# Optimization experiments

Hardware: AMD Instinct MI355X
Metric: run time of the kernel (lower is better)

Reference implementation:

```python
import jax, jax.numpy as jnp
import numpy as np

B, S, DMODEL = 1, 2048, 4096
H, HKV, DH = 32, 8, 128
LTAB, RBKT = 20, 128
NEG = -1e9


def rotate_half(x):
    x1, x2 = x[..., : x.shape[-1] // 2], x[..., x.shape[-1] // 2:]
    return jnp.concatenate((-x2, x1), axis=-1)


def setup_inputs() -> dict:
    key = jax.random.key(0)
    ks = jax.random.split(key, 12)
    inp = {
        "hidden_states": jax.random.normal(ks[0], (B, S, DMODEL), jnp.float32),
        "cos": jax.random.uniform(ks[1], (B, S, DH), jnp.float32),
        "sin": jax.random.uniform(ks[2], (B, S, DH), jnp.float32),
        "q_probs": jax.random.uniform(ks[3], (B, H, LTAB, RBKT), jnp.float32),
        "v_norm": jax.random.uniform(ks[4], (B, H, S), jnp.float32),
        "allowed": jnp.ones((B, H, S), dtype=bool),
        "k_hard": jax.random.randint(ks[5], (B, H, LTAB, S), 0, RBKT, jnp.int32),
        "Wq": jax.random.normal(ks[6], (DMODEL, H * DH), jnp.float32) * 0.02,
        "Wk": jax.random.normal(ks[7], (DMODEL, HKV * DH), jnp.float32) * 0.02,
        "Wv": jax.random.normal(ks[8], (DMODEL, HKV * DH), jnp.float32) * 0.02,
        "Wo": jax.random.normal(ks[9], (H * DH, DMODEL), jnp.float32) * 0.02,
        "sink": 4,
        "window": 128,
        "M": 256,
    }
    return inp


def _sparse_key_mask(q_probs, v_norm, allowed, k_hard, sink, window, M):
    """Faithful jax version of build_sparse_list_decode, returned as a boolean
    allowed-key mask [B, H, T] (equivalent to scattering sparse_list)."""
    Bm, Hm, _, T = k_hard.shape
    # soft-hash collision score: sum over tables of q bucket prob at key's bucket,
    # weighted by value-norm history, restricted to allowed keys.
    coll = jnp.take_along_axis(q_probs, k_hard.astype(jnp.int32), axis=-1).sum(axis=2)  # [B,H,T]
    scores = jnp.where(allowed, coll * v_norm, -jnp.inf)
    M_eff = min(M, T)
    mask = jnp.zeros((Bm, Hm, T), dtype=bool)
    if M_eff > 0:
        heavy_idx = jax.lax.top_k(scores, M_eff)[1]  # [B,H,M]
        b_ix = jnp.arange(Bm)[:, None, None]
        h_ix = jnp.arange(Hm)[None, :, None]
        mask = mask.at[b_ix, h_ix, heavy_idx].set(True)
    sink = max(0, min(sink, T))
    window = max(0, min(window, T))
    if sink > 0:
        mask = mask.at[:, :, :sink].set(True)
    if window > 0:
        win_start = max(T - window, sink)
        if win_start < T:
            mask = mask.at[:, :, win_start:].set(True)
    if sink == 0 and window == 0:
        mask = mask.at[:, :, T - 1].set(True)
    return mask & allowed


def reference(hidden_states, cos, sin, q_probs, v_norm, allowed, k_hard,
              Wq, Wk, Wv, Wo, sink, window, M):
    Bx, Sx, _ = hidden_states.shape
    scaling = DH ** -0.5
    q = (hidden_states @ Wq).reshape(Bx, Sx, H, DH).transpose(0, 2, 1, 3)   # [B,H,S,Dh]
    k = (hidden_states @ Wk).reshape(Bx, Sx, HKV, DH).transpose(0, 2, 1, 3)  # [B,Hkv,S,Dh]
    v = (hidden_states @ Wv).reshape(Bx, Sx, HKV, DH).transpose(0, 2, 1, 3)
    # RoPE (unsqueeze_dim=1)
    c, s = cos[:, None, :, :], sin[:, None, :, :]
    q = q * c + rotate_half(q) * s
    k = k * c + rotate_half(k) * s
    # repeat_kv for GQA
    n_rep = H // HKV
    k = jnp.repeat(k, n_rep, axis=1)
    v = jnp.repeat(v, n_rep, axis=1)
    # sparse heavy-hitter + sink + window key mask (no_grad in the original)
    key_mask = _sparse_key_mask(q_probs, v_norm, allowed, k_hard, sink, window, M)  # [B,H,S]
    causal = jnp.tril(jnp.ones((Sx, Sx), dtype=bool))
    allow = causal[None, None] & key_mask[:, :, None, :]  # [B,H,S,S]
    scores = jnp.einsum('bhqd,bhkd->bhqk', q, k) * scaling
    attn = jax.nn.softmax(jnp.where(allow, scores, NEG), axis=-1)
    out = jnp.einsum('bhqk,bhkd->bhqd', attn, v)
    out = out.transpose(0, 2, 1, 3).reshape(Bx, Sx, H * DH)
    return out @ Wo
```

## Files before the change

### kernel.cpp

```cpp
#include <hip/hip_runtime.h>
#include <hip/hip_bf16.h>
#include <cstdint>
#include <cstddef>

namespace {

constexpr int S_LEN = 2048;
constexpr int DM    = 4096;
constexpr int NH    = 32;
constexpr int NKV   = 8;
constexpr int DH    = 128;
constexpr int LTAB  = 20;
constexpr int RBKT  = 128;
constexpr int NQKV  = NH * DH + 2 * NKV * DH;
constexpr int KOFF  = NH * DH;
constexpr int VOFF  = NH * DH + NKV * DH;

typedef short s16x8 __attribute__((ext_vector_type(8)));
typedef float f32x4 __attribute__((ext_vector_type(4)));
typedef unsigned long long u64;
struct u64x2 { u64 x, y; };

__device__ inline short bf16s(float f) {
  __hip_bfloat16 b = __float2bfloat16(f);
  return (short)*reinterpret_cast<unsigned short*>(&b);
}
__device__ inline float s2f(short s) {
  unsigned short u = (unsigned short)s;
  return __bfloat162float(*reinterpret_cast<__hip_bfloat16*>(&u));
}

__global__ __launch_bounds__(256) void prep_kernel(const float* __restrict__ hidden,
                                                   const float* __restrict__ Wq,
                                                   const float* __restrict__ Wk,
                                                   const float* __restrict__ Wv,
                                                   const float* __restrict__ Wo,
                                                   __hip_bfloat16* __restrict__ hbf,
                                                   __hip_bfloat16* __restrict__ WqkvT,
                                                   __hip_bfloat16* __restrict__ WoT) {
  __shared__ float tile[64][65];
  const int b = blockIdx.x, tid = threadIdx.x;
  if (b < 2048) {
    const size_t base = (size_t)b * 1024;
#pragma unroll
    for (int it = 0; it < 4; ++it) {
      const size_t i = base + it * 256 + tid;
      float4 v = reinterpret_cast<const float4*>(hidden)[i];
      ushort4 o;
      o.x = (unsigned short)bf16s(v.x);
      o.y = (unsigned short)bf16s(v.y);
      o.z = (unsigned short)bf16s(v.z);
      o.w = (unsigned short)bf16s(v.w);
      reinterpret_cast<ushort4*>(hbf)[i] = o;
    }
    return;
  }
  const float* W;
  __hip_bfloat16* Wt;
  int N, bx, by;
  int t = b - 2048;
  if (t < 4096) {
    W = Wq; Wt = WqkvT; N = DM; bx = t & 63; by = t >> 6;
  } else if (t < 5120) {
    t -= 4096; W = Wk; Wt = WqkvT + (size_t)KOFF * DM; N = NKV * DH; bx = t & 15; by = t >> 4;
  } else if (t < 6144) {
    t -= 5120; W = Wv; Wt = WqkvT + (size_t)VOFF * DM; N = NKV * DH; bx = t & 15; by = t >> 4;
  } else {
    t -= 6144; W = Wo; Wt = WoT; N = DM; bx = t & 63; by = t >> 6;
  }
  const int K = DM;
  const int kb = by * 64, nb = bx * 64;
  const int r0 = tid >> 4, c4 = (tid & 15) * 4;
#pragma unroll
  for (int it = 0; it < 4; ++it) {
    const int r = r0 + it * 16;
    float4 v = *reinterpret_cast<const float4*>(&W[(size_t)(kb + r) * N + nb + c4]);
    tile[r][c4] = v.x;
    tile[r][c4 + 1] = v.y;
    tile[r][c4 + 2] = v.z;
    tile[r][c4 + 3] = v.w;
  }
  __syncthreads();
  const int n0 = tid >> 4, k4 = (tid & 15) * 4;
#pragma unroll
  for (int it = 0; it < 4; ++it) {
    const int n = n0 + it * 16;
    ushort4 o;
    o.x = (unsigned short)bf16s(tile[k4][n]);
    o.y = (unsigned short)bf16s(tile[k4 + 1][n]);
    o.z = (unsigned short)bf16s(tile[k4 + 2][n]);
    o.w = (unsigned short)bf16s(tile[k4 + 3][n]);
    *reinterpret_cast<ushort4*>(&Wt[(size_t)(nb + n) * K + kb + k4]) = o;
  }
}

template <bool OUT_F32>
__global__ __launch_bounds__(256) void gemm_bt(const __hip_bfloat16* __restrict__ A,
                                               const __hip_bfloat16* __restrict__ Bt,
                                               void* __restrict__ Cout,
                                               int N, int K) {
  __shared__ __hip_bfloat16 As[128 * 64];
  __shared__ __hip_bfloat16 Bs[128 * 64];
  const int tid = threadIdx.x;
  const int wid = tid >> 6;
  const int lane = tid & 63;
  const int bm = blockIdx.y, bn = blockIdx.x;
  const int wr = wid >> 1, wc = wid & 1;
  f32x4 acc[4][4] = {};
  const __hip_bfloat16* Abase = A + (size_t)bm * 128 * K;
  const __hip_bfloat16* Bbase = Bt + (size_t)bn * 128 * K;
  for (int kt = 0; kt < K; kt += 64) {
    __syncthreads();
#pragma unroll
    for (int j = 0; j < 4; ++j) {
      const int pb = j * 4096 + wid * 1024;
      const int p = pb + lane * 16;
      const int row = p >> 7;
      const int slot = ((p >> 4) & 7) ^ (row & 7);
      const int goff = row * K + kt + slot * 8;
      __builtin_amdgcn_global_load_lds(
          (const __attribute__((address_space(1))) void*)(Abase + goff),
          (__attribute__((address_space(3))) void*)(As + (pb >> 1)), 16, 0, 0);
      __builtin_amdgcn_global_load_lds(
          (const __attribute__((address_space(1))) void*)(Bbase + goff),
          (__attribute__((address_space(3))) void*)(Bs + (pb >> 1)), 16, 0, 0);
    }
    __syncthreads();
#pragma unroll
    for (int kk = 0; kk < 2; ++kk) {
      s16x8 af[4], bf[4];
#pragma unroll
      for (int i = 0; i < 4; ++i) {
        const int ra = wr * 64 + i * 16 + (lane & 15);
        const int sa = (kk * 4 + (lane >> 4)) ^ (ra & 7);
        af[i] = *reinterpret_cast<const s16x8*>(As + ra * 64 + sa * 8);
        const int rb = wc * 64 + i * 16 + (lane & 15);
        const int sb = (kk * 4 + (lane >> 4)) ^ (rb & 7);
        bf[i] = *reinterpret_cast<const s16x8*>(Bs + rb * 64 + sb * 8);
      }
#pragma unroll
      for (int i = 0; i < 4; ++i)
#pragma unroll
        for (int jn = 0; jn < 4; ++jn)
          acc[i][jn] = __builtin_amdgcn_mfma_f32_16x16x32_bf16(af[i], bf[jn], acc[i][jn], 0, 0, 0);
    }
  }
  const int rg = (lane >> 4) * 4;
  const int cg = lane & 15;
#pragma unroll
  for (int i = 0; i < 4; ++i)
#pragma unroll
    for (int jn = 0; jn < 4; ++jn)
#pragma unroll
      for (int r = 0; r < 4; ++r) {
        const int rr = bm * 128 + wr * 64 + i * 16 + rg + r;
        const int cc = bn * 128 + wc * 64 + jn * 16 + cg;
        if (OUT_F32)
          reinterpret_cast<float*>(Cout)[(size_t)rr * N + cc] = acc[i][jn][r];
        else
          reinterpret_cast<__hip_bfloat16*>(Cout)[(size_t)rr * N + cc] =
              __float2bfloat16(acc[i][jn][r]);
      }
}

__global__ __launch_bounds__(256) void rope_kernel(const __hip_bfloat16* __restrict__ QKV,
                                                   const float* __restrict__ cosb,
                                                   const float* __restrict__ sinb,
                                                   __hip_bfloat16* __restrict__ Qro,
                                                   __hip_bfloat16* __restrict__ Kro) {
  const int s = blockIdx.x;
  const int tid = threadIdx.x;
  const float* cs = cosb + s * DH;
  const float* sn = sinb + s * DH;
  const __hip_bfloat16* row = QKV + (size_t)s * NQKV;
  for (int ch = tid; ch < 512 + 128; ch += 256) {
    const bool isQ = ch < 512;
    const int idx8 = (isQ ? ch : ch - 512) * 8;
    const int d8 = idx8 & (DH - 1);
    const int hb = idx8 - d8;
    const __hip_bfloat16* src = isQ ? row : row + KOFF;
    s16x8 v = *reinterpret_cast<const s16x8*>(src + idx8);
    s16x8 p = *reinterpret_cast<const s16x8*>(src + hb + (d8 ^ 64));
    const float sgn = (d8 < 64) ? -1.f : 1.f;
    s16x8 outv;
#pragma unroll
    for (int j = 0; j < 8; ++j) {
      const float r = s2f(v[j]) * cs[d8 + j] + sgn * s2f(p[j]) * sn[d8 + j];
      outv[j] = bf16s(r);
    }
    if (isQ)
      *reinterpret_cast<s16x8*>(Qro + (size_t)s * (NH * DH) + idx8) = outv;
    else
      *reinterpret_cast<s16x8*>(Kro + (size_t)s * (NKV * DH) + idx8) = outv;
  }
}

__global__ __launch_bounds__(1024) void select_kernel(const float* __restrict__ q_probs,
                                                      const float* __restrict__ v_norm,
                                                      const int* __restrict__ allowed,
                                                      const int* __restrict__ k_hard,
                                                      const int* __restrict__ sinkp,
                                                      const int* __restrict__ winp,
                                                      const int* __restrict__ Mp,
                                                      int* __restrict__ sel_idx,
                                                      int* __restrict__ sel_cnt) {
  const int h = blockIdx.x;
  const int tid = threadIdx.x;
  const int lane = tid & 63;
  const int wid = tid >> 6;
  __shared__ u64 keys[S_LEN];
  __shared__ int waveTot[16];
  const int t0 = tid * 2;
  float c0 = 0.f, c1 = 0.f;
#pragma unroll
  for (int l = 0; l < LTAB; ++l) {
    const int2 kh = *reinterpret_cast<const int2*>(&k_hard[(size_t)(h * LTAB + l) * S_LEN + t0]);
    c0 += q_probs[(h * LTAB + l) * RBKT + kh.x];
    c1 += q_probs[(h * LTAB + l) * RBKT + kh.y];
  }
  const int2 al = *reinterpret_cast<const int2*>(&allowed[h * S_LEN + t0]);
  const float2 vn = *reinterpret_cast<const float2*>(&v_norm[h * S_LEN + t0]);
  const float s0 = al.x ? c0 * vn.x : -INFINITY;
  const float s1 = al.y ? c1 * vn.y : -INFINITY;
  auto mkkey = [](float s, int t) -> u64 {
    unsigned m = __float_as_uint(s);
    m = (m & 0x80000000u) ? ~m : (m | 0x80000000u);
    return ((u64)m << 11) | (u64)(S_LEN - 1 - t);
  };
  const u64 k0 = mkkey(s0, t0);
  const u64 k1 = mkkey(s1, t0 + 1);
  keys[t0] = k0;
  keys[t0 + 1] = k1;
  __syncthreads();
  int r0 = 0, r1 = 0;
#pragma unroll 8
  for (int u = 0; u < S_LEN; u += 2) {
    const u64x2 kv = *reinterpret_cast<const u64x2*>(&keys[u]);
    r0 += (kv.x > k0) + (kv.y > k0);
    r1 += (kv.x > k1) + (kv.y > k1);
  }
  const int Mv = min(Mp[0], S_LEN);
  int sv = sinkp[0];
  sv = sv < 0 ? 0 : (sv > S_LEN ? S_LEN : sv);
  int wv = winp[0];
  wv = wv < 0 ? 0 : (wv > S_LEN ? S_LEN : wv);
  int wstart = S_LEN - wv;
  if (wstart < sv) wstart = sv;
  bool sel0 = r0 < Mv, sel1 = r1 < Mv;
  if (t0 < sv) sel0 = true;
  if (t0 + 1 < sv) sel1 = true;
  if (wv > 0) {
    if (t0 >= wstart) sel0 = true;
    if (t0 + 1 >= wstart) sel1 = true;
  }
  if (sv == 0 && wv == 0) {
    if (t0 == S_LEN - 1) sel0 = true;
    if (t0 + 1 == S_LEN - 1) sel1 = true;
  }
  sel0 = sel0 && (al.x != 0);
  sel1 = sel1 && (al.y != 0);
  const int cnt = (sel0 ? 1 : 0) + (sel1 ? 1 : 0);
  int inc = cnt;
#pragma unroll
  for (int off = 1; off < 64; off <<= 1) {
    int n = __shfl_up(inc, off);
    if (lane >= off) inc += n;
  }
  if (lane == 63) waveTot[wid] = inc;
  __syncthreads();
  int wbase = 0;
  for (int w = 0; w < wid; ++w) wbase += waveTot[w];
  int pos = wbase + inc - cnt;
  if (tid == 0) {
    int tot = 0;
#pragma unroll
    for (int w = 0; w < 16; ++w) tot += waveTot[w];
    sel_cnt[h] = tot;
  }
  if (sel0) sel_idx[h * S_LEN + pos++] = t0;
  if (sel1) sel_idx[h * S_LEN + pos] = t0 + 1;
}

__global__ __launch_bounds__(256) void attn_kernel(const __hip_bfloat16* __restrict__ Qro,
                                                   const __hip_bfloat16* __restrict__ Kro,
                                                   const __hip_bfloat16* __restrict__ Vpk,
                                                   const int* __restrict__ sel_idx,
                                                   const int* __restrict__ sel_cnt,
                                                   __hip_bfloat16* __restrict__ ctx) {
  constexpr int BKV = 64;
  const int h = blockIdx.y;
  const int q0 = blockIdx.x * 64;
  const int tid = threadIdx.x, wid = tid >> 6, lane = tid & 63;
  const int l15 = lane & 15, hi = lane >> 4;
  const int kv = h >> 2;
  __shared__ __hip_bfloat16 Ks[BKV][DH + 8];
  __shared__ __hip_bfloat16 Vt[DH][BKV + 8];
  __shared__ __hip_bfloat16 Ps[4][16][BKV + 8];
  __shared__ int tIdx[BKV];
  const int qbase = q0 + wid * 16;
  const float scaling = 0.08838834764831845f;
  s16x8 qf[4];
  {
    const __hip_bfloat16* qp =
        Qro + (size_t)(qbase + l15) * (NH * DH) + h * DH + hi * 8;
#pragma unroll
    for (int kt = 0; kt < 4; ++kt) {
      s16x8 q = *reinterpret_cast<const s16x8*>(qp + kt * 32);
#pragma unroll
      for (int j = 0; j < 8; ++j) q[j] = bf16s(s2f(q[j]) * scaling);
      qf[kt] = q;
    }
  }
  s16x8 ones;
#pragma unroll
  for (int j = 0; j < 8; ++j) ones[j] = (short)0x3F80;
  float mr[4], lr[4];
#pragma unroll
  for (int r = 0; r < 4; ++r) {
    mr[r] = -3.0e38f;
    lr[r] = 0.f;
  }
  f32x4 o[8] = {};
  const int cnt = sel_cnt[h];
  const int qmax = q0 + 63;
  for (int j0 = 0; j0 < cnt; j0 += BKV) {
    if (sel_idx[h * S_LEN + j0] > qmax) break;
    const int nk = min(BKV, cnt - j0);
    __syncthreads();
    if (tid < BKV) tIdx[tid] = (tid < nk) ? sel_idx[h * S_LEN + j0 + tid] : 0x7fffffff;
#pragma unroll
    for (int c = 0; c < 4; ++c) {
      const int ch = tid + c * 256;
      const int row = ch >> 4, c8 = ch & 15;
      if (row < nk) {
        const int t = sel_idx[h * S_LEN + j0 + row];
        *reinterpret_cast<s16x8*>(&Ks[row][c8 * 8]) = *reinterpret_cast<const s16x8*>(
            Kro + (size_t)t * (NKV * DH) + kv * DH + c8 * 8);
      }
    }
    {
      const int j = tid >> 2;
      const int dp = (tid & 3) * 32;
      const int ccA = j ^ (((dp >> 4) & 7) << 3);
      const int ccB = j ^ ((((dp >> 4) + 1) & 7) << 3);
      if (j < nk) {
        const int t = sel_idx[h * S_LEN + j0 + j];
        const __hip_bfloat16* vp = Vpk + (size_t)t * NQKV + kv * DH + dp;
        s16x8 a = *reinterpret_cast<const s16x8*>(vp);
        s16x8 bq = *reinterpret_cast<const s16x8*>(vp + 8);
        s16x8 cq = *reinterpret_cast<const s16x8*>(vp + 16);
        s16x8 dq = *reinterpret_cast<const s16x8*>(vp + 24);
#pragma unroll
        for (int i = 0; i < 8; ++i) reinterpret_cast<short&>(Vt[dp + i][ccA]) = a[i];
#pragma unroll
        for (int i = 0; i < 8; ++i) reinterpret_cast<short&>(Vt[dp + 8 + i][ccA]) = bq[i];
#pragma unroll
        for (int i = 0; i < 8; ++i) reinterpret_cast<short&>(Vt[dp + 16 + i][ccB]) = cq[i];
#pragma unroll
        for (int i = 0; i < 8; ++i) reinterpret_cast<short&>(Vt[dp + 24 + i][ccB]) = dq[i];
      } else {
#pragma unroll
        for (int i = 0; i < 16; ++i) reinterpret_cast<short&>(Vt[dp + i][ccA]) = 0;
#pragma unroll
        for (int i = 0; i < 16; ++i) reinterpret_cast<short&>(Vt[dp + 16 + i][ccB]) = 0;
      }
    }
    __syncthreads();
    f32x4 sc[4];
#pragma unroll
    for (int kc = 0; kc < 4; ++kc) sc[kc] = f32x4{0.f, 0.f, 0.f, 0.f};
#pragma unroll
    for (int kt = 0; kt < 4; ++kt) {
#pragma unroll
      for (int kc = 0; kc < 4; ++kc) {
        const s16x8 kf =
            *reinterpret_cast<const s16x8*>(&Ks[kc * 16 + l15][kt * 32 + hi * 8]);
        sc[kc] = __builtin_amdgcn_mfma_f32_16x16x32_bf16(qf[kt], kf, sc[kc], 0, 0, 0);
      }
    }
    int tt[4];
#pragma unroll
    for (int kc = 0; kc < 4; ++kc) tt[kc] = tIdx[kc * 16 + l15];
    float vv[4][4];
    bool need = false;
#pragma unroll
    for (int r = 0; r < 4; ++r) {
      const int qs = qbase + (hi << 2) + r;
      float mx = -3.0e38f;
#pragma unroll
      for (int kc = 0; kc < 4; ++kc) {
        vv[kc][r] = (tt[kc] <= qs) ? sc[kc][r] : -1.0e9f;
        mx = fmaxf(mx, vv[kc][r]);
      }
      need = need || (mx > mr[r] + 8.f);
    }
    if (__any(need)) {
#pragma unroll
      for (int r = 0; r < 4; ++r) {
        float m = fmaxf(fmaxf(vv[0][r], vv[1][r]), fmaxf(vv[2][r], vv[3][r]));
#pragma unroll
        for (int off = 1; off < 16; off <<= 1) m = fmaxf(m, __shfl_xor(m, off));
        const float mn = fmaxf(mr[r], m);
        const float scl = __expf(mr[r] - mn);
        lr[r] *= scl;
#pragma unroll
        for (int nt = 0; nt < 8; ++nt) o[nt][r] *= scl;
        mr[r] = mn;
      }
    }
#pragma unroll
    for (int r = 0; r < 4; ++r) {
#pragma unroll
      for (int kc = 0; kc < 4; ++kc) {
        Ps[wid][(hi << 2) + r][kc * 16 + l15] = __float2bfloat16(__expf(vv[kc][r] - mr[r]));
      }
    }
    const s16x8 pf0 = *reinterpret_cast<const s16x8*>(&Ps[wid][l15][hi * 8]);
    const s16x8 pf1 = *reinterpret_cast<const s16x8*>(&Ps[wid][l15][32 + hi * 8]);
    {
      f32x4 zero = {0.f, 0.f, 0.f, 0.f};
      f32x4 ps = __builtin_amdgcn_mfma_f32_16x16x32_bf16(pf0, ones, zero, 0, 0, 0);
      ps = __builtin_amdgcn_mfma_f32_16x16x32_bf16(pf1, ones, ps, 0, 0, 0);
#pragma unroll
      for (int r = 0; r < 4; ++r) lr[r] += ps[r];
    }
#pragma unroll
    for (int nt = 0; nt < 8; ++nt) {
      const s16x8 vfa =
          *reinterpret_cast<const s16x8*>(&Vt[nt * 16 + l15][(hi * 8) ^ (nt * 8)]);
      const s16x8 vfb =
          *reinterpret_cast<const s16x8*>(&Vt[nt * 16 + l15][(32 + hi * 8) ^ (nt * 8)]);
      o[nt] = __builtin_amdgcn_mfma_f32_16x16x32_bf16(pf0, vfa, o[nt], 0, 0, 0);
      o[nt] = __builtin_amdgcn_mfma_f32_16x16x32_bf16(pf1, vfb, o[nt], 0, 0, 0);
    }
  }
#pragma unroll
  for (int nt = 0; nt < 8; ++nt)
#pragma unroll
    for (int r = 0; r < 4; ++r) {
      const int qs = qbase + (hi << 2) + r;
      const int d = nt * 16 + l15;
      ctx[(size_t)qs * (NH * DH) + h * DH + d] = __float2bfloat16(o[nt][r] / lr[r]);
    }
}

}

extern "C" void kernel_launch(void* const* d_in, const int* in_sizes, int n_in,
                              void* d_out, int out_size, void* d_ws, size_t ws_size,
                              hipStream_t stream) {
  const float* hidden = (const float*)d_in[0];
  const float* cosb = (const float*)d_in[1];
  const float* sinb = (const float*)d_in[2];
  const float* q_probs = (const float*)d_in[3];
  const float* v_norm = (const float*)d_in[4];
  const int* allowed = (const int*)d_in[5];
  const int* k_hard = (const int*)d_in[6];
  const float* Wq = (const float*)d_in[7];
  const float* Wk = (const float*)d_in[8];
  const float* Wv = (const float*)d_in[9];
  const float* Wo = (const float*)d_in[10];
  const int* sinkp = (const int*)d_in[11];
  const int* winp = (const int*)d_in[12];
  const int* Mp = (const int*)d_in[13];

  char* ws = (char*)d_ws;
  size_t off = 0;
  auto alloc = [&](size_t bytes) -> char* {
    char* p = ws + off;
    off += (bytes + 255) & ~(size_t)255;
    return p;
  };
  __hip_bfloat16* hbf = (__hip_bfloat16*)alloc((size_t)S_LEN * DM * 2);
  __hip_bfloat16* WqkvT = (__hip_bfloat16*)alloc((size_t)NQKV * DM * 2);
  __hip_bfloat16* WoT = (__hip_bfloat16*)alloc((size_t)DM * DM * 2);
  __hip_bfloat16* QKV = (__hip_bfloat16*)alloc((size_t)S_LEN * NQKV * 2);
  __hip_bfloat16* Qro = (__hip_bfloat16*)alloc((size_t)S_LEN * NH * DH * 2);
  __hip_bfloat16* Kro = (__hip_bfloat16*)alloc((size_t)S_LEN * NKV * DH * 2);
  __hip_bfloat16* ctx = (__hip_bfloat16*)alloc((size_t)S_LEN * NH * DH * 2);
  int* sel_idx = (int*)alloc((size_t)NH * S_LEN * 4);
  int* sel_cnt = (int*)alloc((size_t)NH * 4);
  if (off > ws_size) return;

  prep_kernel<<<12288, 256, 0, stream>>>(hidden, Wq, Wk, Wv, Wo, hbf, WqkvT, WoT);

  gemm_bt<false><<<dim3(NQKV / 128, S_LEN / 128), 256, 0, stream>>>(
      hbf, WqkvT, (void*)QKV, NQKV, DM);

  rope_kernel<<<S_LEN, 256, 0, stream>>>(QKV, cosb, sinb, Qro, Kro);

  select_kernel<<<NH, 1024, 0, stream>>>(q_probs, v_norm, allowed, k_hard, sinkp, winp, Mp,
                                         sel_idx, sel_cnt);

  attn_kernel<<<dim3(S_LEN / 64, NH), 256, 0, stream>>>(Qro, Kro, QKV + VOFF, sel_idx,
                                                        sel_cnt, ctx);

  gemm_bt<true><<<dim3(DM / 128, S_LEN / 128), 256, 0, stream>>>(ctx, WoT, d_out, DM, DM);
}
```

Measured before the change: 387.7 us.

## Fuse top-k selection into prep kernel and split-K the output projection

The per-head heavy-hitter selection moves into extra blocks of the prep kernel, with 8 keys per thread in 256-thread blocks, so the separate select launch goes away and the selection overlaps the weight conversion. The output projection GEMM becomes a two-way split-K kernel that writes fp32 partials into the workspace region of the no-longer-needed hidden and QKV weight buffers. A reduce kernel then sums the partials. This doubles the block count for the final GEMM to improve occupancy, at the cost of writing and re-reading 64MB of partials.

Result: no change. 385.6 us (-0.5%).

```diff
diff --git a/kernel.cpp b/kernel.cpp
--- a/kernel.cpp
+++ b/kernel.cpp
@@ -30,18 +30,98 @@
   return __bfloat162float(*reinterpret_cast<__hip_bfloat16*>(&u));
 }
 
-__global__ __launch_bounds__(256) void prep_kernel(const float* __restrict__ hidden,
-                                                   const float* __restrict__ Wq,
-                                                   const float* __restrict__ Wk,
-                                                   const float* __restrict__ Wv,
-                                                   const float* __restrict__ Wo,
-                                                   __hip_bfloat16* __restrict__ hbf,
-                                                   __hip_bfloat16* __restrict__ WqkvT,
-                                                   __hip_bfloat16* __restrict__ WoT) {
+__global__ __launch_bounds__(256) void prep_kernel(
+    const float* __restrict__ hidden, const float* __restrict__ Wq,
+    const float* __restrict__ Wk, const float* __restrict__ Wv,
+    const float* __restrict__ Wo, __hip_bfloat16* __restrict__ hbf,
+    __hip_bfloat16* __restrict__ WqkvT, __hip_bfloat16* __restrict__ WoT,
+    const float* __restrict__ q_probs, const float* __restrict__ v_norm,
+    const int* __restrict__ allowed, const int* __restrict__ k_hard,
+    const int* __restrict__ sinkp, const int* __restrict__ winp,
+    const int* __restrict__ Mp, int* __restrict__ sel_idx, int* __restrict__ sel_cnt) {
   __shared__ float tile[64][65];
+  __shared__ u64 keys[S_LEN];
+  __shared__ int waveTot[4];
   const int b = blockIdx.x, tid = threadIdx.x;
-  if (b < 2048) {
-    const size_t base = (size_t)b * 1024;
+  if (b < 32) {
+    const int h = b;
+    const int lane = tid & 63, wv4 = tid >> 6;
+    const int t0 = tid * 8;
+    float cs[8] = {0.f, 0.f, 0.f, 0.f, 0.f, 0.f, 0.f, 0.f};
+#pragma unroll
+    for (int l = 0; l < LTAB; ++l) {
+      const int* kb = &k_hard[(size_t)(h * LTAB + l) * S_LEN + t0];
+      const int4 ka = *reinterpret_cast<const int4*>(kb);
+      const int4 kc = *reinterpret_cast<const int4*>(kb + 4);
+      const float* qp = &q_probs[(h * LTAB + l) * RBKT];
+      cs[0] += qp[ka.x]; cs[1] += qp[ka.y]; cs[2] += qp[ka.z]; cs[3] += qp[ka.w];
+      cs[4] += qp[kc.x]; cs[5] += qp[kc.y]; cs[6] += qp[kc.z]; cs[7] += qp[kc.w];
+    }
+    const int4 alA = *reinterpret_cast<const int4*>(&allowed[h * S_LEN + t0]);
+    const int4 alB = *reinterpret_cast<const int4*>(&allowed[h * S_LEN + t0 + 4]);
+    const float4 vnA = *reinterpret_cast<const float4*>(&v_norm[h * S_LEN + t0]);
+    const float4 vnB = *reinterpret_cast<const float4*>(&v_norm[h * S_LEN + t0 + 4]);
+    const int al[8] = {alA.x, alA.y, alA.z, alA.w, alB.x, alB.y, alB.z, alB.w};
+    const float vn[8] = {vnA.x, vnA.y, vnA.z, vnA.w, vnB.x, vnB.y, vnB.z, vnB.w};
+    auto mkkey = [](float s, int t) -> u64 {
+      unsigned m = __float_as_uint(s);
+      m = (m & 0x80000000u) ? ~m : (m | 0x80000000u);
+      return ((u64)m << 11) | (u64)(S_LEN - 1 - t);
+    };
+    u64 kk[8];
+#pragma unroll
+    for (int c = 0; c < 8; ++c) {
+      const float sc = al[c] ? cs[c] * vn[c] : -INFINITY;
+      kk[c] = mkkey(sc, t0 + c);
+      keys[t0 + c] = kk[c];
+    }
+    __syncthreads();
+    int rk[8] = {0, 0, 0, 0, 0, 0, 0, 0};
+#pragma unroll 4
+    for (int u = 0; u < S_LEN; u += 2) {
+      const u64x2 kv = *reinterpret_cast<const u64x2*>(&keys[u]);
+#pragma unroll
+      for (int c = 0; c < 8; ++c) rk[c] += (kv.x > kk[c]) + (kv.y > kk[c]);
+    }
+    const int Mv = min(Mp[0], S_LEN);
+    int sv = sinkp[0];
+    sv = sv < 0 ? 0 : (sv > S_LEN ? S_LEN : sv);
+    int wvv = winp[0];
+    wvv = wvv < 0 ? 0 : (wvv > S_LEN ? S_LEN : wvv);
+    int wstart = S_LEN - wvv;
+    if (wstart < sv) wstart = sv;
+    bool sel[8];
+    int cnt = 0;
+#pragma unroll
+    for (int c = 0; c < 8; ++c) {
+      const int t = t0 + c;
+      bool s = rk[c] < Mv;
+      if (t < sv) s = true;
+      if (wvv > 0 && t >= wstart) s = true;
+      if (sv == 0 && wvv == 0 && t == S_LEN - 1) s = true;
+      s = s && (al[c] != 0);
+      sel[c] = s;
+      cnt += s ? 1 : 0;
+    }
+    int inc = cnt;
+#pragma unroll
+    for (int off = 1; off < 64; off <<= 1) {
+      int n = __shfl_up(inc, off);
+      if (lane >= off) inc += n;
+    }
+    if (lane == 63) waveTot[wv4] = inc;
+    __syncthreads();
+    int wbase = 0;
+    for (int w = 0; w < wv4; ++w) wbase += waveTot[w];
+    int pos = wbase + inc - cnt;
+    if (tid == 0) sel_cnt[h] = waveTot[0] + waveTot[1] + waveTot[2] + waveTot[3];
+#pragma unroll
+    for (int c = 0; c < 8; ++c)
+      if (sel[c]) sel_idx[h * S_LEN + pos++] = t0 + c;
+    return;
+  }
+  if (b < 32 + 2048) {
+    const size_t base = (size_t)(b - 32) * 1024;
 #pragma unroll
     for (int it = 0; it < 4; ++it) {
       const size_t i = base + it * 256 + tid;
@@ -58,7 +138,7 @@
   const float* W;
   __hip_bfloat16* Wt;
   int N, bx, by;
-  int t = b - 2048;
+  int t = b - 2080;
   if (t < 4096) {
     W = Wq; Wt = WqkvT; N = DM; bx = t & 63; by = t >> 6;
   } else if (t < 5120) {
@@ -161,6 +241,85 @@
           reinterpret_cast<__hip_bfloat16*>(Cout)[(size_t)rr * N + cc] =
               __float2bfloat16(acc[i][jn][r]);
       }
+}
+
+__global__ __launch_bounds__(256) void gemm_bt_splitk(const __hip_bfloat16* __restrict__ A,
+                                                      const __hip_bfloat16* __restrict__ Bt,
+                                                      float* __restrict__ P,
+                                                      int N, int Kfull, int KH) {
+  __shared__ __hip_bfloat16 As[128 * 64];
+  __shared__ __hip_bfloat16 Bs[128 * 64];
+  const int tid = threadIdx.x;
+  const int wid = tid >> 6;
+  const int lane = tid & 63;
+  const int bm = blockIdx.y, bn = blockIdx.x, kz = blockIdx.z;
+  const int wr = wid >> 1, wc = wid & 1;
+  f32x4 acc[4][4] = {};
+  const __hip_bfloat16* Abase = A + (size_t)bm * 128 * Kfull + kz * KH;
+  const __hip_bfloat16* Bbase = Bt + (size_t)bn * 128 * Kfull + kz * KH;
+  for (int kt = 0; kt < KH; kt += 64) {
+    __syncthreads();
+#pragma unroll
+    for (int j = 0; j < 4; ++j) {
+      const int pb = j * 4096 + wid * 1024;
+      const int p = pb + lane * 16;
+      const int row = p >> 7;
+      const int slot = ((p >> 4) & 7) ^ (row & 7);
+      const int goff = row * Kfull + kt + slot * 8;
+      __builtin_amdgcn_global_load_lds(
+          (const __attribute__((address_space(1))) void*)(Abase + goff),
+          (__attribute__((address_space(3))) void*)(As + (pb >> 1)), 16, 0, 0);
+      __builtin_amdgcn_global_load_lds(
+          (const __attribute__((address_space(1))) void*)(Bbase + goff),
+          (__attribute__((address_space(3))) void*)(Bs + (pb >> 1)), 16, 0, 0);
+    }
+    __syncthreads();
+#pragma unroll
+    for (int kk = 0; kk < 2; ++kk) {
+      s16x8 af[4], bf[4];
+#pragma unroll
+      for (int i = 0; i < 4; ++i) {
+        const int ra = wr * 64 + i * 16 + (lane & 15);
+        const int sa = (kk * 4 + (lane >> 4)) ^ (ra & 7);
+        af[i] = *reinterpret_cast<const s16x8*>(As + ra * 64 + sa * 8);
+        const int rb = wc * 64 + i * 16 + (lane & 15);
+        const int sb = (kk * 4 + (lane >> 4)) ^ (rb & 7);
+        bf[i] = *reinterpret_cast<const s16x8*>(Bs + rb * 64 + sb * 8);
+      }
+#pragma unroll
+      for (int i = 0; i < 4; ++i)
+#pragma unroll
+        for (int jn = 0; jn < 4; ++jn)
+          acc[i][jn] = __builtin_amdgcn_mfma_f32_16x16x32_bf16(af[i], bf[jn], acc[i][jn], 0, 0, 0);
+    }
+  }
+  float* Pz = P + (size_t)kz * S_LEN * N;
+  const int rg = (lane >> 4) * 4;
+  const int cg = lane & 15;
+#pragma unroll
+  for (int i = 0; i < 4; ++i)
+#pragma unroll
+    for (int jn = 0; jn < 4; ++jn)
+#pragma unroll
+      for (int r = 0; r < 4; ++r) {
+        const int rr = bm * 128 + wr * 64 + i * 16 + rg + r;
+        const int cc = bn * 128 + wc * 64 + jn * 16 + cg;
+        Pz[(size_t)rr * N + cc] = acc[i][jn][r];
+      }
+}
+
+__global__ __launch_bounds__(256) void reduce_splitk(const float* __restrict__ P,
+                                                     float* __restrict__ out, int n4) {
+  const int i = blockIdx.x * 256 + threadIdx.x;
+  if (i >= n4) return;
+  const float4 a = reinterpret_cast<const float4*>(P)[i];
+  const float4 b = reinterpret_cast<const float4*>(P + (size_t)S_LEN * DM)[i];
+  float4 o;
+  o.x = a.x + b.x;
+  o.y = a.y + b.y;
+  o.z = a.z + b.z;
+  o.w = a.w + b.w;
+  reinterpret_cast<float4*>(out)[i] = o;
 }
 
 __global__ __launch_bounds__(256) void rope_kernel(const __hip_bfloat16* __restrict__ QKV,
@@ -193,92 +352,6 @@
     else
       *reinterpret_cast<s16x8*>(Kro + (size_t)s * (NKV * DH) + idx8) = outv;
   }
-}
-
-__global__ __launch_bounds__(1024) void select_kernel(const float* __restrict__ q_probs,
-                                                      const float* __restrict__ v_norm,
-                                                      const int* __restrict__ allowed,
-                                                      const int* __restrict__ k_hard,
-                                                      const int* __restrict__ sinkp,
-                                                      const int* __restrict__ winp,
-                                                      const int* __restrict__ Mp,
-                                                      int* __restrict__ sel_idx,
-                                                      int* __restrict__ sel_cnt) {
-  const int h = blockIdx.x;
-  const int tid = threadIdx.x;
-  const int lane = tid & 63;
-  const int wid = tid >> 6;
-  __shared__ u64 keys[S_LEN];
-  __shared__ int waveTot[16];
-  const int t0 = tid * 2;
-  float c0 = 0.f, c1 = 0.f;
-#pragma unroll
-  for (int l = 0; l < LTAB; ++l) {
-    const int2 kh = *reinterpret_cast<const int2*>(&k_hard[(size_t)(h * LTAB + l) * S_LEN + t0]);
-    c0 += q_probs[(h * LTAB + l) * RBKT + kh.x];
-    c1 += q_probs[(h * LTAB + l) * RBKT + kh.y];
-  }
-  const int2 al = *reinterpret_cast<const int2*>(&allowed[h * S_LEN + t0]);
-  const float2 vn = *reinterpret_cast<const float2*>(&v_norm[h * S_LEN + t0]);
-  const float s0 = al.x ? c0 * vn.x : -INFINITY;
-  const float s1 = al.y ? c1 * vn.y : -INFINITY;
-  auto mkkey = [](float s, int t) -> u64 {
-    unsigned m = __float_as_uint(s);
-    m = (m & 0x80000000u) ? ~m : (m | 0x80000000u);
-    return ((u64)m << 11) | (u64)(S_LEN - 1 - t);
-  };
-  const u64 k0 = mkkey(s0, t0);
-  const u64 k1 = mkkey(s1, t0 + 1);
-  keys[t0] = k0;
-  keys[t0 + 1] = k1;
-  __syncthreads();
-  int r0 = 0, r1 = 0;
-#pragma unroll 8
-  for (int u = 0; u < S_LEN; u += 2) {
-    const u64x2 kv = *reinterpret_cast<const u64x2*>(&keys[u]);
-    r0 += (kv.x > k0) + (kv.y > k0);
-    r1 += (kv.x > k1) + (kv.y > k1);
-  }
-  const int Mv = min(Mp[0], S_LEN);
-  int sv = sinkp[0];
-  sv = sv < 0 ? 0 : (sv > S_LEN ? S_LEN : sv);
-  int wv = winp[0];
-  wv = wv < 0 ? 0 : (wv > S_LEN ? S_LEN : wv);
-  int wstart = S_LEN - wv;
-  if (wstart < sv) wstart = sv;
-  bool sel0 = r0 < Mv, sel1 = r1 < Mv;
-  if (t0 < sv) sel0 = true;
-  if (t0 + 1 < sv) sel1 = true;
-  if (wv > 0) {
-    if (t0 >= wstart) sel0 = true;
-    if (t0 + 1 >= wstart) sel1 = true;
-  }
-  if (sv == 0 && wv == 0) {
-    if (t0 == S_LEN - 1) sel0 = true;
-    if (t0 + 1 == S_LEN - 1) sel1 = true;
-  }
-  sel0 = sel0 && (al.x != 0);
-  sel1 = sel1 && (al.y != 0);
-  const int cnt = (sel0 ? 1 : 0) + (sel1 ? 1 : 0);
-  int inc = cnt;
-#pragma unroll
-  for (int off = 1; off < 64; off <<= 1) {
-    int n = __shfl_up(inc, off);
-    if (lane >= off) inc += n;
-  }
-  if (lane == 63) waveTot[wid] = inc;
-  __syncthreads();
-  int wbase = 0;
-  for (int w = 0; w < wid; ++w) wbase += waveTot[w];
-  int pos = wbase + inc - cnt;
-  if (tid == 0) {
-    int tot = 0;
-#pragma unroll
-    for (int w = 0; w < 16; ++w) tot += waveTot[w];
-    sel_cnt[h] = tot;
-  }
-  if (sel0) sel_idx[h * S_LEN + pos++] = t0;
-  if (sel1) sel_idx[h * S_LEN + pos] = t0 + 1;
 }
 
 __global__ __launch_bounds__(256) void attn_kernel(const __hip_bfloat16* __restrict__ Qro,
@@ -481,19 +554,23 @@
   int* sel_idx = (int*)alloc((size_t)NH * S_LEN * 4);
   int* sel_cnt = (int*)alloc((size_t)NH * 4);
   if (off > ws_size) return;
-
-  prep_kernel<<<12288, 256, 0, stream>>>(hidden, Wq, Wk, Wv, Wo, hbf, WqkvT, WoT);
+  float* Psplit = (float*)hbf;
+
+  prep_kernel<<<12320, 256, 0, stream>>>(hidden, Wq, Wk, Wv, Wo, hbf, WqkvT, WoT, q_probs,
+                                         v_norm, allowed, k_hard, sinkp, winp, Mp, sel_idx,
+                                         sel_cnt);
 
   gemm_bt<false><<<dim3(NQKV / 128, S_LEN / 128), 256, 0, stream>>>(
       hbf, WqkvT, (void*)QKV, NQKV, DM);
 
   rope_kernel<<<S_LEN, 256, 0, stream>>>(QKV, cosb, sinb, Qro, Kro);
 
-  select_kernel<<<NH, 1024, 0, stream>>>(q_probs, v_norm, allowed, k_hard, sinkp, winp, Mp,
-                                         sel_idx, sel_cnt);
-
   attn_kernel<<<dim3(S_LEN / 64, NH), 256, 0, stream>>>(Qro, Kro, QKV + VOFF, sel_idx,
                                                         sel_cnt, ctx);
 
-  gemm_bt<true><<<dim3(DM / 128, S_LEN / 128), 256, 0, stream>>>(ctx, WoT, d_out, DM, DM);
-}
+  gemm_bt_splitk<<<dim3(DM / 128, S_LEN / 128, 2), 256, 0, stream>>>(ctx, WoT, Psplit, DM,
+                                                                     DM, DM / 2);
+  reduce_splitk<<<(S_LEN * DM / 4 + 255) / 256, 256, 0, stream>>>((const float*)Psplit,
+                                                                  (float*)d_out,
+                                                                  S_LEN * DM / 4);
+}
```

## Split output projection GEMM over K with fp32 partials and reduce

Applied to the files above, without the earlier changes.

The final Wo projection becomes a two-way split-K GEMM. Each half writes fp32 partials into a scratch area that reuses the dead hidden and WqkvT buffers, and a separate elementwise kernel sums the halves into the output. The goal is to double the number of blocks so the CUs stay busier during the output projection. The cost is roughly twice the output size in extra fp32 write and read traffic, plus one more launch. select_kernel is also launched earlier, and the transpose body is moved into a helper.

Result: slower. 409.4 us (+5.6%).

```diff
diff --git a/kernel.cpp b/kernel.cpp
--- a/kernel.cpp
+++ b/kernel.cpp
@@ -30,14 +30,39 @@
   return __bfloat162float(*reinterpret_cast<__hip_bfloat16*>(&u));
 }
 
-__global__ __launch_bounds__(256) void prep_kernel(const float* __restrict__ hidden,
-                                                   const float* __restrict__ Wq,
-                                                   const float* __restrict__ Wk,
-                                                   const float* __restrict__ Wv,
-                                                   const float* __restrict__ Wo,
-                                                   __hip_bfloat16* __restrict__ hbf,
-                                                   __hip_bfloat16* __restrict__ WqkvT,
-                                                   __hip_bfloat16* __restrict__ WoT) {
+__device__ inline void transpose64_body(const float* __restrict__ W,
+                                        __hip_bfloat16* __restrict__ Wt, int N, int bx,
+                                        int by, int tid, float (*tile)[65]) {
+  const int kb = by * 64, nb = bx * 64;
+  const int r0 = tid >> 4, c4 = (tid & 15) * 4;
+#pragma unroll
+  for (int it = 0; it < 4; ++it) {
+    const int r = r0 + it * 16;
+    float4 v = *reinterpret_cast<const float4*>(&W[(size_t)(kb + r) * N + nb + c4]);
+    tile[r][c4] = v.x;
+    tile[r][c4 + 1] = v.y;
+    tile[r][c4 + 2] = v.z;
+    tile[r][c4 + 3] = v.w;
+  }
+  __syncthreads();
+  const int n0 = tid >> 4, k4 = (tid & 15) * 4;
+#pragma unroll
+  for (int it = 0; it < 4; ++it) {
+    const int n = n0 + it * 16;
+    ushort4 o;
+    o.x = (unsigned short)bf16s(tile[k4][n]);
+    o.y = (unsigned short)bf16s(tile[k4 + 1][n]);
+    o.z = (unsigned short)bf16s(tile[k4 + 2][n]);
+    o.w = (unsigned short)bf16s(tile[k4 + 3][n]);
+    *reinterpret_cast<ushort4*>(&Wt[(size_t)(nb + n) * DM + kb + k4]) = o;
+  }
+}
+
+__global__ __launch_bounds__(256) void prep_kernel(
+    const float* __restrict__ hidden, const float* __restrict__ Wq,
+    const float* __restrict__ Wk, const float* __restrict__ Wv,
+    const float* __restrict__ Wo, __hip_bfloat16* __restrict__ hbf,
+    __hip_bfloat16* __restrict__ WqkvT, __hip_bfloat16* __restrict__ WoT) {
   __shared__ float tile[64][65];
   const int b = blockIdx.x, tid = threadIdx.x;
   if (b < 2048) {
@@ -68,30 +93,93 @@
   } else {
     t -= 6144; W = Wo; Wt = WoT; N = DM; bx = t & 63; by = t >> 6;
   }
-  const int K = DM;
-  const int kb = by * 64, nb = bx * 64;
-  const int r0 = tid >> 4, c4 = (tid & 15) * 4;
-#pragma unroll
-  for (int it = 0; it < 4; ++it) {
-    const int r = r0 + it * 16;
-    float4 v = *reinterpret_cast<const float4*>(&W[(size_t)(kb + r) * N + nb + c4]);
-    tile[r][c4] = v.x;
-    tile[r][c4 + 1] = v.y;
-    tile[r][c4 + 2] = v.z;
-    tile[r][c4 + 3] = v.w;
-  }
+  transpose64_body(W, Wt, N, bx, by, tid, tile);
+}
+
+__global__ __launch_bounds__(1024) void select_kernel(const float* __restrict__ q_probs,
+                                                      const float* __restrict__ v_norm,
+                                                      const int* __restrict__ allowed,
+                                                      const int* __restrict__ k_hard,
+                                                      const int* __restrict__ sinkp,
+                                                      const int* __restrict__ winp,
+                                                      const int* __restrict__ Mp,
+                                                      int* __restrict__ sel_idx,
+                                                      int* __restrict__ sel_cnt) {
+  const int h = blockIdx.x;
+  const int tid = threadIdx.x;
+  const int lane = tid & 63;
+  const int wid = tid >> 6;
+  __shared__ u64 keys[S_LEN];
+  __shared__ int waveTot[16];
+  const int t0 = tid * 2;
+  float c0 = 0.f, c1 = 0.f;
+#pragma unroll
+  for (int l = 0; l < LTAB; ++l) {
+    const int2 kh = *reinterpret_cast<const int2*>(&k_hard[(size_t)(h * LTAB + l) * S_LEN + t0]);
+    c0 += q_probs[(h * LTAB + l) * RBKT + kh.x];
+    c1 += q_probs[(h * LTAB + l) * RBKT + kh.y];
+  }
+  const int2 al = *reinterpret_cast<const int2*>(&allowed[h * S_LEN + t0]);
+  const float2 vn = *reinterpret_cast<const float2*>(&v_norm[h * S_LEN + t0]);
+  const float s0 = al.x ? c0 * vn.x : -INFINITY;
+  const float s1 = al.y ? c1 * vn.y : -INFINITY;
+  auto mkkey = [](float s, int t) -> u64 {
+    unsigned m = __float_as_uint(s);
+    m = (m & 0x80000000u) ? ~m : (m | 0x80000000u);
+    return ((u64)m << 11) | (u64)(S_LEN - 1 - t);
+  };
+  const u64 k0 = mkkey(s0, t0);
+  const u64 k1 = mkkey(s1, t0 + 1);
+  keys[t0] = k0;
+  keys[t0 + 1] = k1;
   __syncthreads();
-  const int n0 = tid >> 4, k4 = (tid & 15) * 4;
-#pragma unroll
-  for (int it = 0; it < 4; ++it) {
-    const int n = n0 + it * 16;
-    ushort4 o;
-    o.x = (unsigned short)bf16s(tile[k4][n]);
-    o.y = (unsigned short)bf16s(tile[k4 + 1][n]);
-    o.z = (unsigned short)bf16s(tile[k4 + 2][n]);
-    o.w = (unsigned short)bf16s(tile[k4 + 3][n]);
-    *reinterpret_cast<ushort4*>(&Wt[(size_t)(nb + n) * K + kb + k4]) = o;
-  }
+  int r0 = 0, r1 = 0;
+#pragma unroll 8
+  for (int u = 0; u < S_LEN; u += 2) {
+    const u64x2 kv = *reinterpret_cast<const u64x2*>(&keys[u]);
+    r0 += (kv.x > k0) + (kv.y > k0);
+    r1 += (kv.x > k1) + (kv.y > k1);
+  }
+  const int Mv = min(Mp[0], S_LEN);
+  int sv = sinkp[0];
+  sv = sv < 0 ? 0 : (sv > S_LEN ? S_LEN : sv);
+  int wv = winp[0];
+  wv = wv < 0 ? 0 : (wv > S_LEN ? S_LEN : wv);
+  int wstart = S_LEN - wv;
+  if (wstart < sv) wstart = sv;
+  bool sel0 = r0 < Mv, sel1 = r1 < Mv;
+  if (t0 < sv) sel0 = true;
+  if (t0 + 1 < sv) sel1 = true;
+  if (wv > 0) {
+    if (t0 >= wstart) sel0 = true;
+    if (t0 + 1 >= wstart) sel1 = true;
+  }
+  if (sv == 0 && wv == 0) {
+    if (t0 == S_LEN - 1) sel0 = true;
+    if (t0 + 1 == S_LEN - 1) sel1 = true;
+  }
+  sel0 = sel0 && (al.x != 0);
+  sel1 = sel1 && (al.y != 0);
+  const int cnt = (sel0 ? 1 : 0) + (sel1 ? 1 : 0);
+  int inc = cnt;
+#pragma unroll
+  for (int off = 1; off < 64; off <<= 1) {
+    int n = __shfl_up(inc, off);
+    if (lane >= off) inc += n;
+  }
+  if (lane == 63) waveTot[wid] = inc;
+  __syncthreads();
+  int wbase = 0;
+  for (int w = 0; w < wid; ++w) wbase += waveTot[w];
+  int pos = wbase + inc - cnt;
+  if (tid == 0) {
+    int tot = 0;
+#pragma unroll
+    for (int w = 0; w < 16; ++w) tot += waveTot[w];
+    sel_cnt[h] = tot;
+  }
+  if (sel0) sel_idx[h * S_LEN + pos++] = t0;
+  if (sel1) sel_idx[h * S_LEN + pos] = t0 + 1;
 }
 
 template <bool OUT_F32>
@@ -161,6 +249,85 @@
           reinterpret_cast<__hip_bfloat16*>(Cout)[(size_t)rr * N + cc] =
               __float2bfloat16(acc[i][jn][r]);
       }
+}
+
+__global__ __launch_bounds__(256) void gemm_bt_splitk(const __hip_bfloat16* __restrict__ A,
+                                                      const __hip_bfloat16* __restrict__ Bt,
+                                                      float* __restrict__ P,
+                                                      int N, int Kfull, int KH) {
+  __shared__ __hip_bfloat16 As[128 * 64];
+  __shared__ __hip_bfloat16 Bs[128 * 64];
+  const int tid = threadIdx.x;
+  const int wid = tid >> 6;
+  const int lane = tid & 63;
+  const int bm = blockIdx.y, bn = blockIdx.x, kz = blockIdx.z;
+  const int wr = wid >> 1, wc = wid & 1;
+  f32x4 acc[4][4] = {};
+  const __hip_bfloat16* Abase = A + (size_t)bm * 128 * Kfull + kz * KH;
+  const __hip_bfloat16* Bbase = Bt + (size_t)bn * 128 * Kfull + kz * KH;
+  for (int kt = 0; kt < KH; kt += 64) {
+    __syncthreads();
+#pragma unroll
+    for (int j = 0; j < 4; ++j) {
+      const int pb = j * 4096 + wid * 1024;
+      const int p = pb + lane * 16;
+      const int row = p >> 7;
+      const int slot = ((p >> 4) & 7) ^ (row & 7);
+      const int goff = row * Kfull + kt + slot * 8;
+      __builtin_amdgcn_global_load_lds(
+          (const __attribute__((address_space(1))) void*)(Abase + goff),
+          (__attribute__((address_space(3))) void*)(As + (pb >> 1)), 16, 0, 0);
+      __builtin_amdgcn_global_load_lds(
+          (const __attribute__((address_space(1))) void*)(Bbase + goff),
+          (__attribute__((address_space(3))) void*)(Bs + (pb >> 1)), 16, 0, 0);
+    }
+    __syncthreads();
+#pragma unroll
+    for (int kk = 0; kk < 2; ++kk) {
+      s16x8 af[4], bf[4];
+#pragma unroll
+      for (int i = 0; i < 4; ++i) {
+        const int ra = wr * 64 + i * 16 + (lane & 15);
+        const int sa = (kk * 4 + (lane >> 4)) ^ (ra & 7);
+        af[i] = *reinterpret_cast<const s16x8*>(As + ra * 64 + sa * 8);
+        const int rb = wc * 64 + i * 16 + (lane & 15);
+        const int sb = (kk * 4 + (lane >> 4)) ^ (rb & 7);
+        bf[i] = *reinterpret_cast<const s16x8*>(Bs + rb * 64 + sb * 8);
+      }
+#pragma unroll
+      for (int i = 0; i < 4; ++i)
+#pragma unroll
+        for (int jn = 0; jn < 4; ++jn)
+          acc[i][jn] = __builtin_amdgcn_mfma_f32_16x16x32_bf16(af[i], bf[jn], acc[i][jn], 0, 0, 0);
+    }
+  }
+  float* Pz = P + (size_t)kz * S_LEN * N;
+  const int rg = (lane >> 4) * 4;
+  const int cg = lane & 15;
+#pragma unroll
+  for (int i = 0; i < 4; ++i)
+#pragma unroll
+    for (int jn = 0; jn < 4; ++jn)
+#pragma unroll
+      for (int r = 0; r < 4; ++r) {
+        const int rr = bm * 128 + wr * 64 + i * 16 + rg + r;
+        const int cc = bn * 128 + wc * 64 + jn * 16 + cg;
+        Pz[(size_t)rr * N + cc] = acc[i][jn][r];
+      }
+}
+
+__global__ __launch_bounds__(256) void reduce_splitk(const float* __restrict__ P,
+                                                     float* __restrict__ out, int n4) {
+  const int i = blockIdx.x * 256 + threadIdx.x;
+  if (i >= n4) return;
+  const float4 a = reinterpret_cast<const float4*>(P)[i];
+  const float4 b = reinterpret_cast<const float4*>(P + (size_t)S_LEN * DM)[i];
+  float4 o;
+  o.x = a.x + b.x;
+  o.y = a.y + b.y;
+  o.z = a.z + b.z;
+  o.w = a.w + b.w;
+  reinterpret_cast<float4*>(out)[i] = o;
 }
 
 __global__ __launch_bounds__(256) void rope_kernel(const __hip_bfloat16* __restrict__ QKV,
@@ -193,92 +360,6 @@
     else
       *reinterpret_cast<s16x8*>(Kro + (size_t)s * (NKV * DH) + idx8) = outv;
   }
-}
-
-__global__ __launch_bounds__(1024) void select_kernel(const float* __restrict__ q_probs,
-                                                      const float* __restrict__ v_norm,
-                                                      const int* __restrict__ allowed,
-                                                      const int* __restrict__ k_hard,
-                                                      const int* __restrict__ sinkp,
-                                                      const int* __restrict__ winp,
-                                                      const int* __restrict__ Mp,
-                                                      int* __restrict__ sel_idx,
-                                                      int* __restrict__ sel_cnt) {
-  const int h = blockIdx.x;
-  const int tid = threadIdx.x;
-  const int lane = tid & 63;
-  const int wid = tid >> 6;
-  __shared__ u64 keys[S_LEN];
-  __shared__ int waveTot[16];
-  const int t0 = tid * 2;
-  float c0 = 0.f, c1 = 0.f;
-#pragma unroll
-  for (int l = 0; l < LTAB; ++l) {
-    const int2 kh = *reinterpret_cast<const int2*>(&k_hard[(size_t)(h * LTAB + l) * S_LEN + t0]);
-    c0 += q_probs[(h * LTAB + l) * RBKT + kh.x];
-    c1 += q_probs[(h * LTAB + l) * RBKT + kh.y];
-  }
-  const int2 al = *reinterpret_cast<const int2*>(&allowed[h * S_LEN + t0]);
-  const float2 vn = *reinterpret_cast<const float2*>(&v_norm[h * S_LEN + t0]);
-  const float s0 = al.x ? c0 * vn.x : -INFINITY;
-  const float s1 = al.y ? c1 * vn.y : -INFINITY;
-  auto mkkey = [](float s, int t) -> u64 {
-    unsigned m = __float_as_uint(s);
-    m = (m & 0x80000000u) ? ~m : (m | 0x80000000u);
-    return ((u64)m << 11) | (u64)(S_LEN - 1 - t);
-  };
-  const u64 k0 = mkkey(s0, t0);
-  const u64 k1 = mkkey(s1, t0 + 1);
-  keys[t0] = k0;
-  keys[t0 + 1] = k1;
-  __syncthreads();
-  int r0 = 0, r1 = 0;
-#pragma unroll 8
-  for (int u = 0; u < S_LEN; u += 2) {
-    const u64x2 kv = *reinterpret_cast<const u64x2*>(&keys[u]);
-    r0 += (kv.x > k0) + (kv.y > k0);
-    r1 += (kv.x > k1) + (kv.y > k1);
-  }
-  const int Mv = min(Mp[0], S_LEN);
-  int sv = sinkp[0];
-  sv = sv < 0 ? 0 : (sv > S_LEN ? S_LEN : sv);
-  int wv = winp[0];
-  wv = wv < 0 ? 0 : (wv > S_LEN ? S_LEN : wv);
-  int wstart = S_LEN - wv;
-  if (wstart < sv) wstart = sv;
-  bool sel0 = r0 < Mv, sel1 = r1 < Mv;
-  if (t0 < sv) sel0 = true;
-  if (t0 + 1 < sv) sel1 = true;
-  if (wv > 0) {
-    if (t0 >= wstart) sel0 = true;
-    if (t0 + 1 >= wstart) sel1 = true;
-  }
-  if (sv == 0 && wv == 0) {
-    if (t0 == S_LEN - 1) sel0 = true;
-    if (t0 + 1 == S_LEN - 1) sel1 = true;
-  }
-  sel0 = sel0 && (al.x != 0);
-  sel1 = sel1 && (al.y != 0);
-  const int cnt = (sel0 ? 1 : 0) + (sel1 ? 1 : 0);
-  int inc = cnt;
-#pragma unroll
-  for (int off = 1; off < 64; off <<= 1) {
-    int n = __shfl_up(inc, off);
-    if (lane >= off) inc += n;
-  }
-  if (lane == 63) waveTot[wid] = inc;
-  __syncthreads();
-  int wbase = 0;
-  for (int w = 0; w < wid; ++w) wbase += waveTot[w];
-  int pos = wbase + inc - cnt;
-  if (tid == 0) {
-    int tot = 0;
-#pragma unroll
-    for (int w = 0; w < 16; ++w) tot += waveTot[w];
-    sel_cnt[h] = tot;
-  }
-  if (sel0) sel_idx[h * S_LEN + pos++] = t0;
-  if (sel1) sel_idx[h * S_LEN + pos] = t0 + 1;
 }
 
 __global__ __launch_bounds__(256) void attn_kernel(const __hip_bfloat16* __restrict__ Qro,
@@ -481,19 +562,24 @@
   int* sel_idx = (int*)alloc((size_t)NH * S_LEN * 4);
   int* sel_cnt = (int*)alloc((size_t)NH * 4);
   if (off > ws_size) return;
+  float* Psplit = (float*)hbf;
 
   prep_kernel<<<12288, 256, 0, stream>>>(hidden, Wq, Wk, Wv, Wo, hbf, WqkvT, WoT);
+
+  select_kernel<<<NH, 1024, 0, stream>>>(q_probs, v_norm, allowed, k_hard, sinkp, winp, Mp,
+                                         sel_idx, sel_cnt);
 
   gemm_bt<false><<<dim3(NQKV / 128, S_LEN / 128), 256, 0, stream>>>(
       hbf, WqkvT, (void*)QKV, NQKV, DM);
 
   rope_kernel<<<S_LEN, 256, 0, stream>>>(QKV, cosb, sinb, Qro, Kro);
 
-  select_kernel<<<NH, 1024, 0, stream>>>(q_probs, v_norm, allowed, k_hard, sinkp, winp, Mp,
-                                         sel_idx, sel_cnt);
-
   attn_kernel<<<dim3(S_LEN / 64, NH), 256, 0, stream>>>(Qro, Kro, QKV + VOFF, sel_idx,
                                                         sel_cnt, ctx);
 
-  gemm_bt<true><<<dim3(DM / 128, S_LEN / 128), 256, 0, stream>>>(ctx, WoT, d_out, DM, DM);
-}
+  gemm_bt_splitk<<<dim3(DM / 128, S_LEN / 128, 2), 256, 0, stream>>>(ctx, WoT, Psplit, DM,
+                                                                     DM, DM / 2);
+  reduce_splitk<<<(S_LEN * DM / 4 + 255) / 256, 256, 0, stream>>>((const float*)Psplit,
+                                                                  (float*)d_out,
+                                                                  S_LEN * DM / 4);
+}
```
